# Optimization experiments

Hardware: AMD Instinct MI355X
Metric: run time of the kernel (lower is better)

## Reference

```python
import jax, jax.numpy as jnp
import numpy as np

H = 1024          # hidden size
NH = 16           # num heads
HD = H // NH      # head dim = 64
I = 4096          # intermediate size
EPS = 1e-5


def _layer_norm(x, g, b):
    m = jnp.mean(x, axis=-1, keepdims=True)
    v = jnp.mean(jnp.square(x - m), axis=-1, keepdims=True)
    return (x - m) * jax.lax.rsqrt(v + EPS) * g + b


def setup_inputs() -> dict:
    key = jax.random.key(0)
    ks = jax.random.split(key, 8)
    B, S = 16, 1025
    s = 0.02
    return {
        "hidden_states": jax.random.normal(ks[0], (B, S, H), dtype=jnp.float32),
        "norm1_g": jnp.ones((H,), jnp.float32),
        "norm1_b": jnp.zeros((H,), jnp.float32),
        "qkv_w": jax.random.normal(ks[1], (3 * H, H), jnp.float32) * s,
        "qkv_b": jnp.zeros((3 * H,), jnp.float32),
        "proj_w": jax.random.normal(ks[2], (H, H), jnp.float32) * s,
        "proj_b": jnp.zeros((H,), jnp.float32),
        "ls1": jnp.full((H,), 0.1, jnp.float32),
        "norm2_g": jnp.ones((H,), jnp.float32),
        "norm2_b": jnp.zeros((H,), jnp.float32),
        "fc1_w": jax.random.normal(ks[3], (I, H), jnp.float32) * s,
        "fc1_b": jnp.zeros((I,), jnp.float32),
        "fc2_w": jax.random.normal(ks[4], (H, I), jnp.float32) * s,
        "fc2_b": jnp.zeros((H,), jnp.float32),
        "ls2": jnp.full((H,), 0.1, jnp.float32),
    }


def reference(hidden_states, norm1_g, norm1_b, qkv_w, qkv_b, proj_w, proj_b,
              ls1, norm2_g, norm2_b, fc1_w, fc1_b, fc2_w, fc2_b, ls2):
    B, S, _ = hidden_states.shape
    scale = HD ** -0.5

    # ---- attention branch ----
    x = _layer_norm(hidden_states, norm1_g, norm1_b)
    qkv = x @ qkv_w.T + qkv_b                      # [B,S,3H]
    qkv = qkv.reshape(B, S, 3, NH, HD).transpose(2, 0, 3, 1, 4)  # [3,B,NH,S,HD]
    q, k, v = qkv[0], qkv[1], qkv[2]
    attn = jnp.einsum('bhqd,bhkd->bhqk', q, k) * scale
    attn = jax.nn.softmax(attn, axis=-1)
    out = jnp.einsum('bhqk,bhkd->bhqd', attn, v)   # [B,NH,S,HD]
    out = out.transpose(0, 2, 1, 3).reshape(B, S, H)
    out = out @ proj_w.T + proj_b
    hidden_states = hidden_states + ls1 * out

    # ---- MLP branch ----
    y = _layer_norm(hidden_states, norm2_g, norm2_b)
    y = jax.nn.gelu(y @ fc1_w.T + fc1_b, approximate=False)
    y = y @ fc2_w.T + fc2_b
    return hidden_states + ls2 * y
```

## Files before the change

kernel.cpp:

```cpp
#include <hip/hip_runtime.h>

typedef __bf16 bf16_t;
typedef bf16_t bf16x8 __attribute__((ext_vector_type(8)));
typedef bf16_t bf16x4 __attribute__((ext_vector_type(4)));
typedef float f32x4 __attribute__((ext_vector_type(4)));

#define S_LEN 1025
#define B_ROWS 1032
#define M_P 16512
#define SP 1152

__global__ __launch_bounds__(256) void cvt_kernel(const float* __restrict__ qkv_w,
                                                  const float* __restrict__ proj_w,
                                                  const float* __restrict__ fc1_w,
                                                  const float* __restrict__ fc2_w,
                                                  bf16_t* __restrict__ out) {
  const int i = blockIdx.x * 256 + threadIdx.x;
  const float* src;
  int j = i;
  if (j < 786432) src = qkv_w;
  else if ((j -= 786432) < 262144) src = proj_w;
  else if ((j -= 262144) < 1048576) src = fc1_w;
  else { j -= 1048576; src = fc2_w; }
  const float4 v = ((const float4*)src)[j];
  bf16x4 o;
  o[0] = (bf16_t)v.x; o[1] = (bf16_t)v.y; o[2] = (bf16_t)v.z; o[3] = (bf16_t)v.w;
  ((bf16x4*)out)[i] = o;
}

__global__ __launch_bounds__(256) void ln_kernel(const float* __restrict__ x,
                                                 const float* __restrict__ g,
                                                 const float* __restrict__ bta,
                                                 bf16_t* __restrict__ o) {
  const int s = blockIdx.x, bb = blockIdx.y;
  const int t = threadIdx.x;
  const float4 v = ((const float4*)(x + ((long)bb * S_LEN + s) * 1024))[t];
  float sm = v.x + v.y + v.z + v.w;
  float sq = v.x * v.x + v.y * v.y + v.z * v.z + v.w * v.w;
#pragma unroll
  for (int off = 32; off > 0; off >>= 1) {
    sm += __shfl_down(sm, off);
    sq += __shfl_down(sq, off);
  }
  __shared__ float red[16];
  const int w = t >> 6, lane = t & 63;
  if (lane == 0) { red[w] = sm; red[8 + w] = sq; }
  __syncthreads();
  if (t == 0) {
    const float ts = red[0] + red[1] + red[2] + red[3];
    const float tq = red[8] + red[9] + red[10] + red[11];
    const float mean = ts * (1.0f / 1024.0f);
    const float var = tq * (1.0f / 1024.0f) - mean * mean;
    red[0] = mean;
    red[1] = rsqrtf(var + 1e-5f);
  }
  __syncthreads();
  const float mean = red[0], rstd = red[1];
  const float4 gg = ((const float4*)g)[t];
  const float4 bb2 = ((const float4*)bta)[t];
  bf16x4 ov;
  ov[0] = (bf16_t)((v.x - mean) * rstd * gg.x + bb2.x);
  ov[1] = (bf16_t)((v.y - mean) * rstd * gg.y + bb2.y);
  ov[2] = (bf16_t)((v.z - mean) * rstd * gg.z + bb2.z);
  ov[3] = (bf16_t)((v.w - mean) * rstd * gg.w + bb2.w);
  ((bf16x4*)(o + ((long)bb * B_ROWS + s) * 1024))[t] = ov;
}

enum { EPI_QKV = 0, EPI_PROJ = 1, EPI_FC2 = 3, EPI_FC1 = 2 };

template <int EPI>
__global__ __launch_bounds__(256) void gemm_bt(const bf16_t* __restrict__ A,
                                               const bf16_t* __restrict__ W,
                                               const float* __restrict__ bias,
                                               const float* __restrict__ resid,
                                               const float* __restrict__ ls,
                                               bf16_t* __restrict__ outb,
                                               float* __restrict__ outf,
                                               bf16_t* __restrict__ vt,
                                               int N, int K, int NT) {
  const int g = blockIdx.x & 7;
  const int rr = blockIdx.x >> 3;
  const int ntile = rr % NT;
  const int mloc = rr / NT;
  const int mtile = g * 17 + mloc;
  if (mtile >= 129) return;
  const int n0 = ntile * 128;
  const int m0 = mtile * 128;

  __shared__ __align__(16) char smem[49152];

  const int t = threadIdx.x;
  const int w = t >> 6;
  const int lane = t & 63;
  const int wm = (w >> 1) * 64;
  const int wn = (w & 1) * 64;
  const int ln = lane & 15;
  const int quad = lane >> 4;

  const f32x4 zero4 = {0.0f, 0.0f, 0.0f, 0.0f};
  f32x4 acc[4][4];
#pragma unroll
  for (int i = 0; i < 4; ++i)
#pragma unroll
    for (int j = 0; j < 4; ++j) acc[i][j] = zero4;

  const int sr0 = t >> 2, sr1 = (t + 256) >> 2;
  const int sc0 = (t & 3) ^ ((sr0 >> 1) & 3);
  const int sc1 = (t & 3) ^ ((sr1 >> 1) & 3);
  const bf16_t* a0 = A + (long)(m0 + sr0) * K + sc0 * 8;
  const bf16_t* a1 = A + (long)(m0 + sr1) * K + sc1 * 8;
  const bf16_t* b0 = W + (long)(n0 + sr0) * K + sc0 * 8;
  const bf16_t* b1 = W + (long)(n0 + sr1) * K + sc1 * 8;

  const int laneOff = ln * 64 + ((quad ^ ((ln >> 1) & 3)) << 4);

#define STAGE(KT, RING)                                                                       \
  {                                                                                           \
    char* dA_ = smem + (RING) * 16384;                                                        \
    char* dB_ = dA_ + 8192;                                                                   \
    __builtin_amdgcn_global_load_lds(                                                         \
        (const __attribute__((address_space(1))) void*)(a0 + (KT)),                           \
        (__attribute__((address_space(3))) void*)(dA_ + t * 16), 16, 0, 0);                   \
    __builtin_amdgcn_global_load_lds(                                                         \
        (const __attribute__((address_space(1))) void*)(a1 + (KT)),                           \
        (__attribute__((address_space(3))) void*)(dA_ + (t + 256) * 16), 16, 0, 0);           \
    __builtin_amdgcn_global_load_lds(                                                         \
        (const __attribute__((address_space(1))) void*)(b0 + (KT)),                           \
        (__attribute__((address_space(3))) void*)(dB_ + t * 16), 16, 0, 0);                   \
    __builtin_amdgcn_global_load_lds(                                                         \
        (const __attribute__((address_space(1))) void*)(b1 + (KT)),                           \
        (__attribute__((address_space(3))) void*)(dB_ + (t + 256) * 16), 16, 0, 0);           \
  }

  STAGE(0, 0)
  STAGE(32, 1)

  const int NTILES = K >> 5;
  int cur = 0;
  for (int T = 0; T < NTILES - 1; ++T) {
    asm volatile("s_waitcnt vmcnt(4)" ::: "memory");
    __builtin_amdgcn_s_barrier();
    __builtin_amdgcn_sched_barrier(0);

    const char* ringA = smem + cur * 16384;
    const char* ringB = ringA + 8192;
    bf16x8 af[4], bfr[4];
#pragma unroll
    for (int mt = 0; mt < 4; ++mt)
      af[mt] = *(const bf16x8*)(ringA + (wm + mt * 16) * 64 + laneOff);
#pragma unroll
    for (int nt = 0; nt < 4; ++nt)
      bfr[nt] = *(const bf16x8*)(ringB + (wn + nt * 16) * 64 + laneOff);

    if (T + 2 < NTILES) {
      const int stg = (cur == 0) ? 2 : cur - 1;
      STAGE((T + 2) * 32, stg)
    }
    __builtin_amdgcn_sched_barrier(0);

    __builtin_amdgcn_s_setprio(1);
#pragma unroll
    for (int mt = 0; mt < 4; ++mt)
#pragma unroll
      for (int nt = 0; nt < 4; ++nt)
        acc[mt][nt] = __builtin_amdgcn_mfma_f32_16x16x32_bf16(af[mt], bfr[nt], acc[mt][nt], 0, 0, 0);
    __builtin_amdgcn_s_setprio(0);
    cur = (cur == 2) ? 0 : cur + 1;
  }
  {
    asm volatile("s_waitcnt vmcnt(0)" ::: "memory");
    __builtin_amdgcn_s_barrier();
    const char* ringA = smem + cur * 16384;
    const char* ringB = ringA + 8192;
    bf16x8 af[4], bfr[4];
#pragma unroll
    for (int mt = 0; mt < 4; ++mt)
      af[mt] = *(const bf16x8*)(ringA + (wm + mt * 16) * 64 + laneOff);
#pragma unroll
    for (int nt = 0; nt < 4; ++nt)
      bfr[nt] = *(const bf16x8*)(ringB + (wn + nt * 16) * 64 + laneOff);
#pragma unroll
    for (int mt = 0; mt < 4; ++mt)
#pragma unroll
      for (int nt = 0; nt < 4; ++nt)
        acc[mt][nt] = __builtin_amdgcn_mfma_f32_16x16x32_bf16(af[mt], bfr[nt], acc[mt][nt], 0, 0, 0);
  }
#undef STAGE
  __syncthreads();

  if (EPI == EPI_PROJ || EPI == EPI_FC2) {
    const int b0r = m0 / B_ROWS;
    const int s0 = m0 - b0r * B_ROWS;
#pragma unroll
    for (int nt = 0; nt < 4; ++nt) {
      const int n = n0 + wn + nt * 16 + ln;
      const float bn = bias[n];
      const float lsn = ls[n];
#pragma unroll
      for (int mt = 0; mt < 4; ++mt) {
#pragma unroll
        for (int r = 0; r < 4; ++r) {
          const int d = wm + mt * 16 + quad * 4 + r;
          int s = s0 + d, b = b0r;
          if (s >= B_ROWS) { s -= B_ROWS; ++b; }
          if (s < S_LEN) {
            const long idx = ((long)b * S_LEN + s) * 1024 + n;
            outf[idx] = resid[idx] + lsn * (acc[mt][nt][r] + bn);
          }
        }
      }
    }
    return;
  }

  if (EPI == EPI_QKV && n0 >= 2048) {
    bf16_t* C = (bf16_t*)smem;
#pragma unroll
    for (int nt = 0; nt < 4; ++nt) {
      const int nl = wn + nt * 16 + ln;
      const float bn = bias[n0 + nl];
#pragma unroll
      for (int mt = 0; mt < 4; ++mt)
#pragma unroll
        for (int r = 0; r < 4; ++r)
          C[nl * 134 + (wm + mt * 16 + quad * 4 + r)] = (bf16_t)(acc[mt][nt][r] + bn);
    }
    __syncthreads();
    const int b0r = m0 / B_ROWS;
    const int s0 = m0 - b0r * B_ROWS;
#pragma unroll
    for (int p = 0; p < 8; ++p) {
      const int nl = p * 16 + (t >> 4);
      const int sc = (t & 15) * 8;
      const int n = n0 + nl;
      const int h = (n >> 6) - 32, d = n & 63;
      int s = s0 + sc, b = b0r;
      if (s >= B_ROWS) { s -= B_ROWS; ++b; }
      *(bf16x8*)&vt[(((long)b * 16 + h) * 64 + d) * (long)SP + s] =
          *(const bf16x8*)&C[nl * 134 + sc];
    }
    return;
  }

  {
    bf16_t* C = (bf16_t*)smem;
#pragma unroll
    for (int nt = 0; nt < 4; ++nt) {
      const int nl = wn + nt * 16 + ln;
      const float bn = bias[n0 + nl];
#pragma unroll
      for (int mt = 0; mt < 4; ++mt)
#pragma unroll
        for (int r = 0; r < 4; ++r) {
          float c = acc[mt][nt][r] + bn;
          if (EPI == EPI_FC1) c = c / (1.0f + __expf(-1.702f * c));
          C[(wm + mt * 16 + quad * 4 + r) * 132 + nl] = (bf16_t)c;
        }
    }
    __syncthreads();
    const long stride = (EPI == EPI_QKV) ? 2048 : N;
#pragma unroll
    for (int p = 0; p < 8; ++p) {
      const int row = p * 16 + (t >> 4);
      const int sc = (t & 15) * 8;
      *(bf16x8*)&outb[(long)(m0 + row) * stride + n0 + sc] = *(const bf16x8*)&C[row * 132 + sc];
    }
  }
}

#define SCL 0.18033688f

__global__ __launch_bounds__(256) void attn_kernel(const bf16_t* __restrict__ qk,
                                                   const bf16_t* __restrict__ vt,
                                                   bf16_t* __restrict__ out) {
  const int g = blockIdx.x & 7;
  const int idx = blockIdx.x >> 3;
  const int bh = g * 32 + idx / 17;
  const int q0 = (idx % 17) * 64;
  const int b = bh >> 4, h = bh & 15;
  const int t = threadIdx.x;
  const int wv = t >> 6, lane = t & 63;
  const int ln = lane & 15, quad = lane >> 4;

  __shared__ __align__(16) char smem[35840];
  bf16_t* ldsK = (bf16_t*)smem;
  bf16_t* ldsP = (bf16_t*)smem;
  bf16_t* ldsV = (bf16_t*)(smem + 18432);

  const long rowbase = (long)b * B_ROWS;

  int qrow = q0 + wv * 16 + ln;
  if (qrow > S_LEN - 1) qrow = S_LEN - 1;
  const bf16_t* qp = qk + (rowbase + qrow) * 2048 + h * 64;
  const bf16x8 qf0 = *(const bf16x8*)(qp + quad * 8);
  const bf16x8 qf1 = *(const bf16x8*)(qp + 32 + quad * 8);

  const bf16_t* vbase = vt + (long)bh * 64 * SP;

  const f32x4 zero4 = {0.0f, 0.0f, 0.0f, 0.0f};
  f32x4 oacc[4];
  float l_part[4] = {0.0f, 0.0f, 0.0f, 0.0f};
#pragma unroll
  for (int i = 0; i < 4; ++i) oacc[i] = zero4;

  for (int k0 = 0; k0 < 1152; k0 += 128) {
    __syncthreads();
#pragma unroll
    for (int i = 0; i < 4; ++i) {
      const int slot = t + i * 256;
      const int key = slot >> 3, ch = (slot & 7) * 8;
      int krow = k0 + key;
      if (krow > S_LEN - 1) krow = S_LEN - 1;
      *(bf16x8*)&ldsK[key * 72 + ch] =
          *(const bf16x8*)(qk + (rowbase + krow) * 2048 + 1024 + h * 64 + ch);
    }
#pragma unroll
    for (int i = 0; i < 4; ++i) {
      const int slot = t + i * 256;
      const int dim = slot >> 4, kc = (slot & 15) * 8;
      *(bf16x8*)&ldsV[dim * 136 + kc] = *(const bf16x8*)(vbase + (long)dim * SP + k0 + kc);
    }
    __syncthreads();

    f32x4 s[8];
#pragma unroll
    for (int nt = 0; nt < 8; ++nt) {
      const bf16x8 kf0 = *(const bf16x8*)&ldsK[(nt * 16 + ln) * 72 + quad * 8];
      const bf16x8 kf1 = *(const bf16x8*)&ldsK[(nt * 16 + ln) * 72 + 32 + quad * 8];
      f32x4 a = zero4;
      a = __builtin_amdgcn_mfma_f32_16x16x32_bf16(qf0, kf0, a, 0, 0, 0);
      a = __builtin_amdgcn_mfma_f32_16x16x32_bf16(qf1, kf1, a, 0, 0, 0);
#pragma unroll
      for (int r = 0; r < 4; ++r) s[nt][r] = a[r] * SCL;
    }
    if (k0 + 128 > S_LEN) {
#pragma unroll
      for (int nt = 0; nt < 8; ++nt) {
        const bool valid = (k0 + nt * 16 + ln) < S_LEN;
#pragma unroll
        for (int r = 0; r < 4; ++r) s[nt][r] = valid ? s[nt][r] : -1e30f;
      }
    }
    __syncthreads();

    bf16_t* P = ldsP + wv * 2176;
#pragma unroll
    for (int nt = 0; nt < 8; ++nt)
#pragma unroll
      for (int r = 0; r < 4; ++r) {
        const float p = exp2f(s[nt][r]);
        l_part[r] += p;
        P[(quad * 4 + r) * 136 + nt * 16 + ln] = (bf16_t)p;
      }

#pragma unroll
    for (int ko = 0; ko < 4; ++ko) {
      const bf16x8 pf = *(const bf16x8*)&P[ln * 136 + ko * 32 + quad * 8];
#pragma unroll
      for (int dt = 0; dt < 4; ++dt) {
        const bf16x8 vf = *(const bf16x8*)&ldsV[(dt * 16 + ln) * 136 + ko * 32 + quad * 8];
        oacc[dt] = __builtin_amdgcn_mfma_f32_16x16x32_bf16(pf, vf, oacc[dt], 0, 0, 0);
      }
    }
  }

#pragma unroll
  for (int off = 1; off < 16; off <<= 1)
#pragma unroll
    for (int r = 0; r < 4; ++r) l_part[r] += __shfl_xor(l_part[r], off);

#pragma unroll
  for (int r = 0; r < 4; ++r) {
    const int q = q0 + wv * 16 + quad * 4 + r;
    if (q < S_LEN) {
      const float inv = 1.0f / l_part[r];
#pragma unroll
      for (int dt = 0; dt < 4; ++dt)
        out[(rowbase + q) * 1024 + h * 64 + dt * 16 + ln] = (bf16_t)(oacc[dt][r] * inv);
    }
  }
}

extern "C" void kernel_launch(void* const* d_in, const int* in_sizes, int n_in,
                              void* d_out, int out_size, void* d_ws, size_t ws_size,
                              hipStream_t stream) {
  (void)in_sizes; (void)n_in; (void)out_size; (void)ws_size;
  const float* hidden = (const float*)d_in[0];
  const float* n1g = (const float*)d_in[1];
  const float* n1b = (const float*)d_in[2];
  const float* qkv_w = (const float*)d_in[3];
  const float* qkv_b = (const float*)d_in[4];
  const float* proj_w = (const float*)d_in[5];
  const float* proj_b = (const float*)d_in[6];
  const float* ls1 = (const float*)d_in[7];
  const float* n2g = (const float*)d_in[8];
  const float* n2b = (const float*)d_in[9];
  const float* fc1_w = (const float*)d_in[10];
  const float* fc1_b = (const float*)d_in[11];
  const float* fc2_w = (const float*)d_in[12];
  const float* fc2_b = (const float*)d_in[13];
  const float* ls2 = (const float*)d_in[14];
  float* out = (float*)d_out;

  char* ws = (char*)d_ws;
  bf16_t* R1 = (bf16_t*)ws;
  char* shared = ws + 33816576L;
  bf16_t* qkbuf = (bf16_t*)shared;
  bf16_t* vtbuf = (bf16_t*)(shared + 67633152L);
  bf16_t* gelu = (bf16_t*)shared;
  bf16_t* wqkv = (bf16_t*)(ws + 33816576L + 135266304L);
  bf16_t* wproj = wqkv + 3145728;
  bf16_t* wfc1 = wproj + 1048576;
  bf16_t* wfc2 = wfc1 + 4194304;

  cvt_kernel<<<12288, 256, 0, stream>>>(qkv_w, proj_w, fc1_w, fc2_w, wqkv);

  ln_kernel<<<dim3(S_LEN, 16), 256, 0, stream>>>(hidden, n1g, n1b, R1);

  gemm_bt<EPI_QKV><<<136 * 24, 256, 0, stream>>>(R1, wqkv, qkv_b, nullptr, nullptr,
                                                 qkbuf, nullptr, vtbuf, 3072, 1024, 24);

  attn_kernel<<<4352, 256, 0, stream>>>(qkbuf, vtbuf, R1);

  gemm_bt<EPI_PROJ><<<136 * 8, 256, 0, stream>>>(R1, wproj, proj_b, hidden, ls1,
                                                 nullptr, out, nullptr, 1024, 1024, 8);

  ln_kernel<<<dim3(S_LEN, 16), 256, 0, stream>>>(out, n2g, n2b, R1);

  gemm_bt<EPI_FC1><<<136 * 32, 256, 0, stream>>>(R1, wfc1, fc1_b, nullptr, nullptr,
                                                 gelu, nullptr, nullptr, 4096, 1024, 32);

  gemm_bt<EPI_FC2><<<136 * 8, 256, 0, stream>>>(gelu, wfc2, fc2_b, out, ls2,
                                                nullptr, out, nullptr, 1024, 4096, 8);
}
```

Before: 1.013 ms.

## Peel last key out of attention loop and fold softmax scale into QKV epilogue

The attention key loop now covers 1024 keys instead of 1152, and the single leftover key (index 1024) is handled with a scalar dot product and a rank-1 update after the loop. This drops one mostly-padded 128-key tile and the masking logic. The softmax scale is applied to Q in the QKV GEMM epilogue instead of to every score. s_setprio is also raised around the MFMA sections. The scale is now applied to Q before the bf16 rounding, which slightly changes numerics.

```diff
diff --git a/kernel.cpp b/kernel.cpp
--- a/kernel.cpp
+++ b/kernel.cpp
@@ -9,6 +9,7 @@
 #define B_ROWS 1032
 #define M_P 16512
 #define SP 1152
+#define SCL 0.18033688f
 
 __global__ __launch_bounds__(256) void cvt_kernel(const float* __restrict__ qkv_w,
                                                   const float* __restrict__ proj_w,
@@ -253,6 +254,9 @@
 #pragma unroll
         for (int r = 0; r < 4; ++r) {
           float c = acc[mt][nt][r] + bn;
+          if (EPI == EPI_QKV) {
+            if (n0 < 1024) c *= SCL;
+          }
           if (EPI == EPI_FC1) c = c / (1.0f + __expf(-1.702f * c));
           C[(wm + mt * 16 + quad * 4 + r) * 132 + nl] = (bf16_t)c;
         }
@@ -267,8 +271,6 @@
     }
   }
 }
-
-#define SCL 0.18033688f
 
 __global__ __launch_bounds__(256) void attn_kernel(const bf16_t* __restrict__ qk,
                                                    const bf16_t* __restrict__ vt,
@@ -303,16 +305,14 @@
 #pragma unroll
   for (int i = 0; i < 4; ++i) oacc[i] = zero4;
 
-  for (int k0 = 0; k0 < 1152; k0 += 128) {
+  for (int k0 = 0; k0 < 1024; k0 += 128) {
     __syncthreads();
 #pragma unroll
     for (int i = 0; i < 4; ++i) {
       const int slot = t + i * 256;
       const int key = slot >> 3, ch = (slot & 7) * 8;
-      int krow = k0 + key;
-      if (krow > S_LEN - 1) krow = S_LEN - 1;
       *(bf16x8*)&ldsK[key * 72 + ch] =
-          *(const bf16x8*)(qk + (rowbase + krow) * 2048 + 1024 + h * 64 + ch);
+          *(const bf16x8*)(qk + (rowbase + k0 + key) * 2048 + 1024 + h * 64 + ch);
     }
 #pragma unroll
     for (int i = 0; i < 4; ++i) {
@@ -323,6 +323,7 @@
     __syncthreads();
 
     f32x4 s[8];
+    __builtin_amdgcn_s_setprio(1);
 #pragma unroll
     for (int nt = 0; nt < 8; ++nt) {
       const bf16x8 kf0 = *(const bf16x8*)&ldsK[(nt * 16 + ln) * 72 + quad * 8];
@@ -330,17 +331,9 @@
       f32x4 a = zero4;
       a = __builtin_amdgcn_mfma_f32_16x16x32_bf16(qf0, kf0, a, 0, 0, 0);
       a = __builtin_amdgcn_mfma_f32_16x16x32_bf16(qf1, kf1, a, 0, 0, 0);
-#pragma unroll
-      for (int r = 0; r < 4; ++r) s[nt][r] = a[r] * SCL;
-    }
-    if (k0 + 128 > S_LEN) {
-#pragma unroll
-      for (int nt = 0; nt < 8; ++nt) {
-        const bool valid = (k0 + nt * 16 + ln) < S_LEN;
-#pragma unroll
-        for (int r = 0; r < 4; ++r) s[nt][r] = valid ? s[nt][r] : -1e30f;
-      }
-    }
+      s[nt] = a;
+    }
+    __builtin_amdgcn_s_setprio(0);
     __syncthreads();
 
     bf16_t* P = ldsP + wv * 2176;
@@ -353,6 +346,7 @@
         P[(quad * 4 + r) * 136 + nt * 16 + ln] = (bf16_t)p;
       }
 
+    __builtin_amdgcn_s_setprio(1);
 #pragma unroll
     for (int ko = 0; ko < 4; ++ko) {
       const bf16x8 pf = *(const bf16x8*)&P[ln * 136 + ko * 32 + quad * 8];
@@ -362,12 +356,39 @@
         oacc[dt] = __builtin_amdgcn_mfma_f32_16x16x32_bf16(pf, vf, oacc[dt], 0, 0, 0);
       }
     }
+    __builtin_amdgcn_s_setprio(0);
   }
 
 #pragma unroll
   for (int off = 1; off < 16; off <<= 1)
 #pragma unroll
     for (int r = 0; r < 4; ++r) l_part[r] += __shfl_xor(l_part[r], off);
+
+  {
+    const bf16_t* kp = qk + (rowbase + 1024) * 2048 + 1024 + h * 64;
+    const bf16x8 kl0 = *(const bf16x8*)(kp + quad * 8);
+    const bf16x8 kl1 = *(const bf16x8*)(kp + 32 + quad * 8);
+    float sl = 0.0f;
+#pragma unroll
+    for (int j = 0; j < 8; ++j)
+      sl += (float)qf0[j] * (float)kl0[j] + (float)qf1[j] * (float)kl1[j];
+    sl += __shfl_xor(sl, 16);
+    sl += __shfl_xor(sl, 32);
+
+    float p_last[4];
+#pragma unroll
+    for (int r = 0; r < 4; ++r)
+      p_last[r] = exp2f(__shfl(sl, quad * 4 + r));
+
+#pragma unroll
+    for (int dt = 0; dt < 4; ++dt) {
+      const float vv = (float)vt[((long)bh * 64 + dt * 16 + ln) * SP + 1024];
+#pragma unroll
+      for (int r = 0; r < 4; ++r) oacc[dt][r] += p_last[r] * vv;
+    }
+#pragma unroll
+    for (int r = 0; r < 4; ++r) l_part[r] += p_last[r];
+  }
 
 #pragma unroll
   for (int r = 0; r < 4; ++r) {
```

New measurement: 967.4 us. 4.5% less time.
